# Kernel tuning notes

Measured on AMD Instinct MI355X. Metric: run time of the kernel, lower is better.

Reference implementation:

```python
import jax, jax.numpy as jnp
import numpy as np

# dims: batch, token counts, feature dims, hidden d, glimpses
B, VN, QN, AN = 16, 96, 96, 96
VD = QD = AD = 256
HD, G = 128, 2
W_STD = 0.02


def setup_inputs() -> dict:
    key = jax.random.key(0)
    ks = jax.random.split(key, 24)
    f32 = jnp.float32
    def w(k, shape):
        return jax.random.normal(k, shape, f32) * W_STD
    return {
        'v': jax.random.normal(ks[0], (B, VN, VD), f32),
        'q': jax.random.normal(ks[1], (B, QN, QD), f32),
        'a': jax.random.normal(ks[2], (B, AN, AD), f32),
        # TCNet tucker projections (FCNet: Linear + ReLU)
        'Wvt': w(ks[3], (VD, HD)), 'bvt': jnp.zeros((HD,), f32),
        'Wqt': w(ks[4], (QD, HD)), 'bqt': jnp.zeros((HD,), f32),
        'Wat': w(ks[5], (AD, HD)), 'bat': jnp.zeros((HD,), f32),
        # trilinear core mapping shared hidden dim -> glimpses
        'Wg': w(ks[6], (HD, G)),
        # value projections (plain Linear, *_dim -> h_dim)
        'Wvp': w(ks[7], (VD, HD)), 'bvp': jnp.zeros((HD,), f32),
        'Wqp': w(ks[8], (QD, HD)), 'bqp': jnp.zeros((HD,), f32),
        'Wap': w(ks[9], (AD, HD)), 'bap': jnp.zeros((HD,), f32),
        # residual updates (glimpse*h_dim -> *_dim)
        'Wvu': w(ks[10], (G * HD, VD)), 'bvu': jnp.zeros((VD,), f32),
        'Wqu': w(ks[11], (G * HD, QD)), 'bqu': jnp.zeros((QD,), f32),
        'Wau': w(ks[12], (G * HD, AD)), 'bau': jnp.zeros((AD,), f32),
    }


def reference(v, q, a,
              Wvt, bvt, Wqt, bqt, Wat, bat, Wg,
              Wvp, bvp, Wqp, bqp, Wap, bap,
              Wvu, bvu, Wqu, bqu, Wau, bau):
    b = v.shape[0]
    # --- TCNet (reconstructed trilinear scorer): tucker proj + rank-1 core ---
    vt = jax.nn.relu(v @ Wvt + bvt)               # [b, vn, h]
    qt = jax.nn.relu(q @ Wqt + bqt)               # [b, qn, h]
    at = jax.nn.relu(a @ Wat + bat)               # [b, an, h]
    logits = jnp.einsum('bvh,bqh,bah,hg->bvqag', vt, qt, at, Wg)
    z = vt.sum(1) * qt.sum(1) * at.sum(1)         # pooled trilinear embedding [b, h]
    # --- mask padded v tokens (rows whose abs-sum is 0), softmax over v*q*a ---
    mask = (jnp.abs(v).sum(2) == 0)[:, :, None, None, None]
    logits = jnp.where(mask, -jnp.inf, logits)
    p = jax.nn.softmax(logits.reshape(b, -1, G), axis=1).reshape(logits.shape)
    # --- value projections + broadcast-sum combinations ---
    vp = v @ Wvp + bvp                            # [b, vn, d]
    qp = q @ Wqp + bqp                            # [b, qn, d]
    ap = a @ Wap + bap                            # [b, an, d]
    qa = qp[:, :, None, :] + ap[:, None, :, :]    # [b, qn, an, d]
    va = vp[:, :, None, :] + ap[:, None, :, :]    # [b, vn, an, d]
    vq = vp[:, :, None, :] + qp[:, None, :, :]    # [b, vn, qn, d]
    # --- three attended contractions + residual linear updates (eval: no dropout) ---
    c_v = jnp.einsum('bvqag,bqad->bvdg', p, qa)
    c_v = jnp.swapaxes(c_v, 2, 3).reshape(b, v.shape[1], G * HD)  # permute(0,1,3,2).view
    updated_v = v + c_v @ Wvu + bvu
    c_q = jnp.einsum('bvqag,bvad->bqdg', p, va)
    c_q = jnp.swapaxes(c_q, 2, 3).reshape(b, q.shape[1], G * HD)
    updated_q = q + c_q @ Wqu + bqu
    c_a = jnp.einsum('bvqag,bvqd->bagd', p, vq)   # note: torch einsum emits [b,a,g,d]
    c_a = jnp.swapaxes(c_a, 2, 3).reshape(b, a.shape[1], HD * G)  # then permute(0,1,3,2).view
    updated_a = a + c_a @ Wau + bau
    return jnp.stack([updated_v, updated_q, updated_a])  # [3, b, n, dim]
```

## Files before the change

kernel.cpp:

```cpp
#include <hip/hip_runtime.h>


#define B_  16
#define N_  96
#define D_  256
#define H_  128
#define CV  4
#define NCH 24
#define PAD 136

typedef _Float16 f16x8 __attribute__((ext_vector_type(8)));
typedef float f32x4_t  __attribute__((ext_vector_type(4)));

__device__ __forceinline__ float bf2f(unsigned short u) {
    union { unsigned u32; float f; } x;
    x.u32 = ((unsigned)u) << 16;
    return x.f;
}

__global__ __launch_bounds__(256) void k_proj(
    const float* __restrict__ v, const float* __restrict__ q,
    const float* __restrict__ a,
    const float* __restrict__ Wvt, const float* __restrict__ bvt,
    const float* __restrict__ Wqt, const float* __restrict__ bqt,
    const float* __restrict__ Wat, const float* __restrict__ bat,
    const float* __restrict__ Wvp, const float* __restrict__ bvp,
    const float* __restrict__ Wqp, const float* __restrict__ bqp,
    const float* __restrict__ Wap, const float* __restrict__ bap,
    const float* __restrict__ Wg,
    _Float16* __restrict__ vtg_o, _Float16* __restrict__ qt_o,
    _Float16* __restrict__ at_o,
    float* __restrict__ vp_o, float* __restrict__ qp_o, float* __restrict__ ap_o)
{
    int wg = blockIdx.x;
    int tc = wg % 8, b = (wg / 8) & 15, p = wg / 128;
    const float* xs_[6] = {v, q, a, v, q, a};
    const float* Ws_[6] = {Wvt, Wqt, Wat, Wvp, Wqp, Wap};
    const float* bs_[6] = {bvt, bqt, bat, bvp, bqp, bap};

    __shared__ __align__(16) float x_l[12 * D_];

    int tid = threadIdx.x;
    int t0 = tc * 12;
    const float* x = xs_[p] + (size_t)(b * N_ + t0) * D_;
    for (int i = tid; i < 768; i += 256)
        ((float4*)x_l)[i] = ((const float4*)x)[i];
    __syncthreads();

    int d = tid & 127, tg = tid >> 7;
    const float* W = Ws_[p];
    float bias = bs_[p][d];
    float acc[6];
#pragma unroll
    for (int t = 0; t < 6; t++) acc[t] = bias;

    for (int kb = 0; kb < 32; kb++) {
        int k = kb * 8;
        float w0 = W[(k + 0) * H_ + d], w1 = W[(k + 1) * H_ + d];
        float w2 = W[(k + 2) * H_ + d], w3 = W[(k + 3) * H_ + d];
        float w4 = W[(k + 4) * H_ + d], w5 = W[(k + 5) * H_ + d];
        float w6 = W[(k + 6) * H_ + d], w7 = W[(k + 7) * H_ + d];
#pragma unroll
        for (int t = 0; t < 6; t++) {
            int lt = tg * 6 + t;
            float4 xa = *(const float4*)&x_l[lt * D_ + k];
            float4 xb = *(const float4*)&x_l[lt * D_ + k + 4];
            acc[t] += xa.x * w0 + xa.y * w1 + xa.z * w2 + xa.w * w3
                    + xb.x * w4 + xb.y * w5 + xb.z * w6 + xb.w * w7;
        }
    }

    int trow = b * N_ + t0 + tg * 6;
    if (p == 0) {
        float wg0 = Wg[d * 2 + 0], wg1 = Wg[d * 2 + 1];
#pragma unroll
        for (int t = 0; t < 6; t++) {
            float r = fmaxf(acc[t], 0.f);
            _Float16* vg = vtg_o + (size_t)(trow + t) * 2 * H_;
            vg[d]      = (_Float16)(r * wg0);
            vg[H_ + d] = (_Float16)(r * wg1);
        }
    } else if (p < 3) {
        _Float16* o = (p == 1) ? qt_o : at_o;
#pragma unroll
        for (int t = 0; t < 6; t++)
            o[(trow + t) * H_ + d] = (_Float16)fmaxf(acc[t], 0.f);
    } else {
        float* outs[3] = {vp_o, qp_o, ap_o};
        float* o = outs[p - 3];
#pragma unroll
        for (int t = 0; t < 6; t++) o[(trow + t) * H_ + d] = acc[t];
    }
}

__global__ __launch_bounds__(256) void k_logits(
    const _Float16* __restrict__ vtg, const _Float16* __restrict__ qt,
    const _Float16* __restrict__ at,
    float* __restrict__ Evq_part, float* __restrict__ Eva_part,
    unsigned short* __restrict__ E_qa_part)
{
    int bid = blockIdx.x;
    int g = bid & 1, vc = (bid >> 1) % NCH, b = bid / (2 * NCH);
    int tid = threadIdx.x;

    __shared__ __align__(16) _Float16 qt_l[N_ * PAD];
    __shared__ __align__(16) _Float16 at_l[N_ * PAD];

    const _Float16* qtb = qt + (size_t)b * N_ * H_;
    const _Float16* atb = at + (size_t)b * N_ * H_;

    for (int it = 0; it < 12; it++) {
        int i = tid + it * 256;
        int e = i * 4, t = e >> 7, h = e & 127;
        *(ushort4*)&qt_l[t * PAD + h] = *(const ushort4*)&qtb[e];
        *(ushort4*)&at_l[t * PAD + h] = *(const ushort4*)&atb[e];
    }
    __syncthreads();

    int wave = tid >> 6, lane = tid & 63, quad = lane >> 4, l15 = lane & 15;
    int qi0 = (wave >> 1) * 3, aj0 = (wave & 1) * 3;

    float eqa[3][3][4];
#pragma unroll
    for (int i = 0; i < 3; i++)
#pragma unroll
        for (int j = 0; j < 3; j++)
#pragma unroll
            for (int r = 0; r < 4; r++) eqa[i][j][r] = 0.f;

    for (int vl = 0; vl < CV; vl++) {
        int vrow = vc * CV + vl;
        const _Float16* vgp = vtg + ((size_t)(b * N_ + vrow) * 2 + g) * H_;

        f32x4_t acc[3][3];
#pragma unroll
        for (int i = 0; i < 3; i++)
#pragma unroll
            for (int j = 0; j < 3; j++)
                acc[i][j] = (f32x4_t){0.f, 0.f, 0.f, 0.f};

#pragma unroll
        for (int ks = 0; ks < 4; ks++) {
            f16x8 v8 = *(const f16x8*)&vgp[ks * 32 + quad * 8];
            f16x8 af[3], bfr[3];
#pragma unroll
            for (int i = 0; i < 3; i++)
                af[i] = *(const f16x8*)&qt_l[((qi0 + i) * 16 + l15) * PAD + ks * 32 + quad * 8];
#pragma unroll
            for (int jt = 0; jt < 3; jt++) {
                f16x8 raw = *(const f16x8*)&at_l[((aj0 + jt) * 16 + l15) * PAD + ks * 32 + quad * 8];
                bfr[jt] = raw * v8;
            }
#pragma unroll
            for (int i = 0; i < 3; i++)
#pragma unroll
                for (int jt = 0; jt < 3; jt++)
                    acc[i][jt] = __builtin_amdgcn_mfma_f32_16x16x32_f16(af[i], bfr[jt], acc[i][jt], 0, 0, 0);
        }

        float s[3][4];
        float c[3];
#pragma unroll
        for (int i = 0; i < 3; i++) {
            s[i][0] = 0.f; s[i][1] = 0.f; s[i][2] = 0.f; s[i][3] = 0.f;
        }
        c[0] = 0.f; c[1] = 0.f; c[2] = 0.f;
#pragma unroll
        for (int i = 0; i < 3; i++)
#pragma unroll
            for (int jt = 0; jt < 3; jt++) {
                float e0 = __expf(fminf(fmaxf(acc[i][jt][0], -30.f), 30.f));
                float e1 = __expf(fminf(fmaxf(acc[i][jt][1], -30.f), 30.f));
                float e2 = __expf(fminf(fmaxf(acc[i][jt][2], -30.f), 30.f));
                float e3 = __expf(fminf(fmaxf(acc[i][jt][3], -30.f), 30.f));
                eqa[i][jt][0] += e0; eqa[i][jt][1] += e1;
                eqa[i][jt][2] += e2; eqa[i][jt][3] += e3;
                s[i][0] += e0; s[i][1] += e1; s[i][2] += e2; s[i][3] += e3;
                c[jt] += e0 + e1 + e2 + e3;
            }

        float* evqp = Evq_part + ((size_t)bid * CV + vl) * 192 + (wave & 1) * 96;
#pragma unroll
        for (int i = 0; i < 3; i++) {
            float s0 = s[i][0], s1 = s[i][1], s2 = s[i][2], s3 = s[i][3];
#pragma unroll
            for (int m = 1; m < 16; m <<= 1) {
                s0 += __shfl_xor(s0, m); s1 += __shfl_xor(s1, m);
                s2 += __shfl_xor(s2, m); s3 += __shfl_xor(s3, m);
            }
            if (l15 == 0) {
                int qr = (qi0 + i) * 16 + quad * 4;
                evqp[qr + 0] = s0; evqp[qr + 1] = s1;
                evqp[qr + 2] = s2; evqp[qr + 3] = s3;
            }
        }
        float* evap = Eva_part + ((size_t)bid * CV + vl) * 192 + (wave >> 1) * 96;
#pragma unroll
        for (int jt = 0; jt < 3; jt++) {
            float cs = c[jt];
            cs += __shfl_xor(cs, 16);
            cs += __shfl_xor(cs, 32);
            if (lane < 16) evap[(aj0 + jt) * 16 + l15] = cs;
        }
    }

    unsigned short* Pp = E_qa_part + (size_t)bid * 9216;
#pragma unroll
    for (int i = 0; i < 3; i++)
#pragma unroll
        for (int jt = 0; jt < 3; jt++)
#pragma unroll
            for (int r = 0; r < 4; r++) {
                int idx = (i * 3 + jt) * 4 + r;
                union { float f; unsigned u; } x;
                x.f = eqa[i][jt][r];
                unsigned rr = x.u + 0x7fffu + ((x.u >> 16) & 1u);
                Pp[idx * 256 + tid] = (unsigned short)(rr >> 16);
            }
}

__global__ __launch_bounds__(256) void k_reduce(
    const unsigned short* __restrict__ E_qa_part, float* __restrict__ E_qa)
{
    int wg = blockIdx.x;
    int idx = wg % 36, bg = wg / 36;
    int b = bg >> 1, g = bg & 1;
    int tid = threadIdx.x;

    float s = 0.f;
    const unsigned short* Pp = E_qa_part + ((size_t)(b * 2 * NCH + g)) * 9216 + idx * 256 + tid;
#pragma unroll
    for (int vc = 0; vc < NCH; vc++) s += bf2f(Pp[(size_t)vc * 2 * 9216]);

    int wave = tid >> 6, lane = tid & 63, quad = lane >> 4, l15 = lane & 15;
    int qi0 = (wave >> 1) * 3, aj0 = (wave & 1) * 3;
    int i = idx / 12, jt = (idx / 4) % 3, r = idx & 3;
    int qq = (qi0 + i) * 16 + quad * 4 + r;
    int aa = (aj0 + jt) * 16 + l15;
    E_qa[(size_t)bg * 9216 + qq * 96 + aa] = s;
}

__global__ __launch_bounds__(256) void k_merge(
    const float* __restrict__ Evq_part, const float* __restrict__ Eva_part,
    float* __restrict__ E_vq, float* __restrict__ E_va, float* __restrict__ Zinv)
{
    int b = blockIdx.x >> 1, g = blockIdx.x & 1;
    int tid = threadIdx.x;
    float z = 0.f;
    for (int i = tid; i < 9216; i += 256) {
        int vrow = i / 96, col = i - vrow * 96;
        int vc = vrow / CV, vl = vrow - vc * CV;
        size_t pb = ((size_t)(b * 2 * NCH + vc * 2 + g) * CV + vl) * 192;
        float s1 = Evq_part[pb + col] + Evq_part[pb + 96 + col];
        E_vq[(b * 2 + g) * 9216 + i] = s1;
        z += s1;
        float s2 = Eva_part[pb + col] + Eva_part[pb + 96 + col];
        E_va[(b * 2 + g) * 9216 + i] = s2;
    }
    __shared__ float red[256];
    red[tid] = z;
    __syncthreads();
    for (int s = 128; s > 0; s >>= 1) {
        if (tid < s) red[tid] += red[tid + s];
        __syncthreads();
    }
    if (tid == 0) Zinv[b * 2 + g] = 1.f / fmaxf(red[0], 1e-30f);
}

__global__ __launch_bounds__(256) void k_ctx(
    const float* __restrict__ E_vq, const float* __restrict__ E_va,
    const float* __restrict__ E_qa,
    const float* __restrict__ vp, const float* __restrict__ qp,
    const float* __restrict__ ap, const float* __restrict__ Zinv,
    float* __restrict__ out)
{
    int wg = blockIdx.x;
    int tc = wg % 6, g = (wg / 6) & 1, b = (wg / 12) & 15, o = wg / 192;
    int tid = threadIdx.x;
    __shared__ __align__(16) float E1l[16 * 100];
    __shared__ __align__(16) float E2l[16 * 100];
    int t0 = tc * 16;
    const float* Evq = E_vq + (b * 2 + g) * 9216;
    const float* Eva = E_va + (b * 2 + g) * 9216;
    const float* Eqa = E_qa + (b * 2 + g) * 9216;

    if (o == 0) {
        for (int i = tid; i < 1536; i += 256) {
            int t = i / 96, j = i - t * 96;
            E1l[t * 100 + j] = Evq[(t0 + t) * 96 + j];
            E2l[t * 100 + j] = Eva[(t0 + t) * 96 + j];
        }
    } else if (o == 1) {
        for (int i = tid; i < 1536; i += 256) {
            int t = i & 15, j = i >> 4;
            E1l[t * 100 + j] = Evq[j * 96 + t0 + t];
        }
        for (int i = tid; i < 1536; i += 256) {
            int t = i / 96, j = i - t * 96;
            E2l[t * 100 + j] = Eqa[(t0 + t) * 96 + j];
        }
    } else {
        for (int i = tid; i < 1536; i += 256) {
            int t = i & 15, j = i >> 4;
            E1l[t * 100 + j] = Eva[j * 96 + t0 + t];
            E2l[t * 100 + j] = Eqa[j * 96 + t0 + t];
        }
    }
    __syncthreads();

    const float* P1 = ((o == 0) ? qp : vp) + b * N_ * H_;
    const float* P2 = ((o == 2) ? qp : ap) + b * N_ * H_;
    int d = tid & 127, tg = tid >> 7;
    float acc[8] = {0.f, 0.f, 0.f, 0.f, 0.f, 0.f, 0.f, 0.f};
    for (int jb = 0; jb < 24; jb++) {
        int j4 = jb * 4;
        float p10 = P1[(j4 + 0) * H_ + d], p11 = P1[(j4 + 1) * H_ + d];
        float p12 = P1[(j4 + 2) * H_ + d], p13 = P1[(j4 + 3) * H_ + d];
        float p20 = P2[(j4 + 0) * H_ + d], p21 = P2[(j4 + 1) * H_ + d];
        float p22 = P2[(j4 + 2) * H_ + d], p23 = P2[(j4 + 3) * H_ + d];
#pragma unroll
        for (int t8 = 0; t8 < 8; t8++) {
            int t = tg * 8 + t8;
            float4 e1 = *(const float4*)&E1l[t * 100 + j4];
            float4 e2 = *(const float4*)&E2l[t * 100 + j4];
            acc[t8] += e1.x * p10 + e1.y * p11 + e1.z * p12 + e1.w * p13
                     + e2.x * p20 + e2.y * p21 + e2.z * p22 + e2.w * p23;
        }
    }
    float zi = Zinv[b * 2 + g];
    float* ob = out + (size_t)((o * B_ + b) * N_) * 256;
#pragma unroll
    for (int t8 = 0; t8 < 8; t8++) {
        int T = t0 + tg * 8 + t8;
        int col = (o == 2) ? (d * 2 + g) : (g * 128 + d);
        ob[T * 256 + col] = acc[t8] * zi;
    }
}

__global__ __launch_bounds__(256) void k_update(
    const float* __restrict__ v, const float* __restrict__ q,
    const float* __restrict__ a,
    const float* __restrict__ Wvu, const float* __restrict__ bvu,
    const float* __restrict__ Wqu, const float* __restrict__ bqu,
    const float* __restrict__ Wau, const float* __restrict__ bau,
    float* __restrict__ out)
{
    int wg = blockIdx.x;
    int tc = wg % 12, b = (wg / 12) & 15, o = wg / 192;
    int tid = threadIdx.x;
    const float* xs_[3] = {v, q, a};
    const float* Ws_[3] = {Wvu, Wqu, Wau};
    const float* bs_[3] = {bvu, bqu, bau};
    int t0 = tc * 8;

    __shared__ __align__(16) float c_l[8 * 256];
    float* cbase = out + (size_t)((o * B_ + b) * N_ + t0) * 256;
    for (int i = tid; i < 2048; i += 256) c_l[i] = cbase[i];
    __syncthreads();

    const float* W = Ws_[o];
    const float* x = xs_[o] + (size_t)(b * N_ + t0) * 256;
    float bias = bs_[o][tid];
    float acc[8];
#pragma unroll
    for (int t = 0; t < 8; t++) acc[t] = bias + x[t * 256 + tid];

    for (int kb = 0; kb < 64; kb++) {
        int k = kb * 4;
        float w0 = W[(k + 0) * 256 + tid];
        float w1 = W[(k + 1) * 256 + tid];
        float w2 = W[(k + 2) * 256 + tid];
        float w3 = W[(k + 3) * 256 + tid];
#pragma unroll
        for (int t = 0; t < 8; t++) {
            float4 c4 = *(const float4*)&c_l[t * 256 + k];
            acc[t] += c4.x * w0 + c4.y * w1 + c4.z * w2 + c4.w * w3;
        }
    }
#pragma unroll
    for (int t = 0; t < 8; t++) cbase[t * 256 + tid] = acc[t];
}

extern "C" void kernel_launch(void* const* d_in, const int* in_sizes, int n_in,
                              void* d_out, int out_size, void* d_ws, size_t ws_size,
                              hipStream_t stream)
{
    const float* v   = (const float*)d_in[0];
    const float* q   = (const float*)d_in[1];
    const float* a   = (const float*)d_in[2];
    const float* Wvt = (const float*)d_in[3];
    const float* bvt = (const float*)d_in[4];
    const float* Wqt = (const float*)d_in[5];
    const float* bqt = (const float*)d_in[6];
    const float* Wat = (const float*)d_in[7];
    const float* bat = (const float*)d_in[8];
    const float* Wg  = (const float*)d_in[9];
    const float* Wvp = (const float*)d_in[10];
    const float* bvp = (const float*)d_in[11];
    const float* Wqp = (const float*)d_in[12];
    const float* bqp = (const float*)d_in[13];
    const float* Wap = (const float*)d_in[14];
    const float* bap = (const float*)d_in[15];
    const float* Wvu = (const float*)d_in[16];
    const float* bvu = (const float*)d_in[17];
    const float* Wqu = (const float*)d_in[18];
    const float* bqu = (const float*)d_in[19];
    const float* Wau = (const float*)d_in[20];
    const float* bau = (const float*)d_in[21];

    char* ws = (char*)d_ws;
    size_t off = 0;
    auto alloc = [&](size_t bytes) {
        char* p = ws + off;
        off += (bytes + 255) & ~(size_t)255;
        return (void*)p;
    };
    _Float16* vtg = (_Float16*)alloc((size_t)B_ * N_ * 2 * H_ * 2);
    _Float16* qt  = (_Float16*)alloc((size_t)B_ * N_ * H_ * 2);
    _Float16* at  = (_Float16*)alloc((size_t)B_ * N_ * H_ * 2);
    float* vpb  = (float*)alloc((size_t)B_ * N_ * H_ * 4);
    float* qpb  = (float*)alloc((size_t)B_ * N_ * H_ * 4);
    float* apb  = (float*)alloc((size_t)B_ * N_ * H_ * 4);
    float* E_vq = (float*)alloc((size_t)B_ * 2 * 9216 * 4);
    float* E_va = (float*)alloc((size_t)B_ * 2 * 9216 * 4);
    float* E_qa = (float*)alloc((size_t)B_ * 2 * 9216 * 4);
    float* Zinv = (float*)alloc(256);
    float* Evq_part = (float*)alloc((size_t)768 * CV * 192 * 4);
    float* Eva_part = (float*)alloc((size_t)768 * CV * 192 * 4);
    unsigned short* E_qa_part =
        (unsigned short*)alloc((size_t)B_ * NCH * 2 * 9216 * 2);

    k_proj<<<768, 256, 0, stream>>>(v, q, a, Wvt, bvt, Wqt, bqt, Wat, bat,
                                    Wvp, bvp, Wqp, bqp, Wap, bap, Wg,
                                    vtg, qt, at, vpb, qpb, apb);
    k_logits<<<B_ * NCH * 2, 256, 0, stream>>>(vtg, qt, at,
                                               Evq_part, Eva_part, E_qa_part);
    k_reduce<<<1152, 256, 0, stream>>>(E_qa_part, E_qa);
    k_merge<<<32, 256, 0, stream>>>(Evq_part, Eva_part, E_vq, E_va, Zinv);
    k_ctx<<<576, 256, 0, stream>>>(E_vq, E_va, E_qa, vpb, qpb, apb, Zinv,
                                   (float*)d_out);
    k_update<<<576, 256, 0, stream>>>(v, q, a, Wvu, bvu, Wqu, bqu, Wau, bau,
                                      (float*)d_out);
}
```

Baseline: 206.1 us.

## Fuse reduce/merge kernels and fuse context contraction into residual update

Merges k_reduce and k_merge into a single k_mid launch that branches on block index. Fuses k_ctx with k_update so each block computes the context for its 8 tokens across both glimpses into shared memory and immediately applies the residual linear layer. This removes two launches and the global round-trip of the context tensor through the output buffer. In exchange, each k_ctxup block now does both contractions serially with a smaller token tile, and the P1/P2 loads are repeated across more blocks.

```diff
diff --git a/kernel.cpp b/kernel.cpp
--- a/kernel.cpp
+++ b/kernel.cpp
@@ -219,125 +219,58 @@
             }
 }
 
-__global__ __launch_bounds__(256) void k_reduce(
-    const unsigned short* __restrict__ E_qa_part, float* __restrict__ E_qa)
+__global__ __launch_bounds__(256) void k_mid(
+    const unsigned short* __restrict__ E_qa_part,
+    const float* __restrict__ Evq_part, const float* __restrict__ Eva_part,
+    float* __restrict__ E_qa, float* __restrict__ E_vq,
+    float* __restrict__ E_va, float* __restrict__ Zinv)
 {
     int wg = blockIdx.x;
-    int idx = wg % 36, bg = wg / 36;
-    int b = bg >> 1, g = bg & 1;
     int tid = threadIdx.x;
-
-    float s = 0.f;
-    const unsigned short* Pp = E_qa_part + ((size_t)(b * 2 * NCH + g)) * 9216 + idx * 256 + tid;
-#pragma unroll
-    for (int vc = 0; vc < NCH; vc++) s += bf2f(Pp[(size_t)vc * 2 * 9216]);
-
-    int wave = tid >> 6, lane = tid & 63, quad = lane >> 4, l15 = lane & 15;
-    int qi0 = (wave >> 1) * 3, aj0 = (wave & 1) * 3;
-    int i = idx / 12, jt = (idx / 4) % 3, r = idx & 3;
-    int qq = (qi0 + i) * 16 + quad * 4 + r;
-    int aa = (aj0 + jt) * 16 + l15;
-    E_qa[(size_t)bg * 9216 + qq * 96 + aa] = s;
-}
-
-__global__ __launch_bounds__(256) void k_merge(
-    const float* __restrict__ Evq_part, const float* __restrict__ Eva_part,
-    float* __restrict__ E_vq, float* __restrict__ E_va, float* __restrict__ Zinv)
-{
-    int b = blockIdx.x >> 1, g = blockIdx.x & 1;
-    int tid = threadIdx.x;
-    float z = 0.f;
-    for (int i = tid; i < 9216; i += 256) {
-        int vrow = i / 96, col = i - vrow * 96;
-        int vc = vrow / CV, vl = vrow - vc * CV;
-        size_t pb = ((size_t)(b * 2 * NCH + vc * 2 + g) * CV + vl) * 192;
-        float s1 = Evq_part[pb + col] + Evq_part[pb + 96 + col];
-        E_vq[(b * 2 + g) * 9216 + i] = s1;
-        z += s1;
-        float s2 = Eva_part[pb + col] + Eva_part[pb + 96 + col];
-        E_va[(b * 2 + g) * 9216 + i] = s2;
-    }
-    __shared__ float red[256];
-    red[tid] = z;
-    __syncthreads();
-    for (int s = 128; s > 0; s >>= 1) {
-        if (tid < s) red[tid] += red[tid + s];
+    if (wg < 1152) {
+        int idx = wg % 36, bg = wg / 36;
+        int b = bg >> 1, g = bg & 1;
+        float s = 0.f;
+        const unsigned short* Pp = E_qa_part + ((size_t)(b * 2 * NCH + g)) * 9216 + idx * 256 + tid;
+#pragma unroll
+        for (int vc = 0; vc < NCH; vc++) s += bf2f(Pp[(size_t)vc * 2 * 9216]);
+
+        int wave = tid >> 6, lane = tid & 63, quad = lane >> 4, l15 = lane & 15;
+        int qi0 = (wave >> 1) * 3, aj0 = (wave & 1) * 3;
+        int i = idx / 12, jt = (idx / 4) % 3, r = idx & 3;
+        int qq = (qi0 + i) * 16 + quad * 4 + r;
+        int aa = (aj0 + jt) * 16 + l15;
+        E_qa[(size_t)bg * 9216 + qq * 96 + aa] = s;
+    } else {
+        int bg = wg - 1152;
+        int b = bg >> 1, g = bg & 1;
+        float z = 0.f;
+        for (int i = tid; i < 9216; i += 256) {
+            int vrow = i / 96, col = i - vrow * 96;
+            int vc = vrow / CV, vl = vrow - vc * CV;
+            size_t pb = ((size_t)(b * 2 * NCH + vc * 2 + g) * CV + vl) * 192;
+            float s1 = Evq_part[pb + col] + Evq_part[pb + 96 + col];
+            E_vq[(b * 2 + g) * 9216 + i] = s1;
+            z += s1;
+            float s2 = Eva_part[pb + col] + Eva_part[pb + 96 + col];
+            E_va[(b * 2 + g) * 9216 + i] = s2;
+        }
+        __shared__ float red[256];
+        red[tid] = z;
         __syncthreads();
-    }
-    if (tid == 0) Zinv[b * 2 + g] = 1.f / fmaxf(red[0], 1e-30f);
-}
-
-__global__ __launch_bounds__(256) void k_ctx(
+        for (int s = 128; s > 0; s >>= 1) {
+            if (tid < s) red[tid] += red[tid + s];
+            __syncthreads();
+        }
+        if (tid == 0) Zinv[b * 2 + g] = 1.f / fmaxf(red[0], 1e-30f);
+    }
+}
+
+__global__ __launch_bounds__(256) void k_ctxup(
     const float* __restrict__ E_vq, const float* __restrict__ E_va,
     const float* __restrict__ E_qa,
     const float* __restrict__ vp, const float* __restrict__ qp,
     const float* __restrict__ ap, const float* __restrict__ Zinv,
-    float* __restrict__ out)
-{
-    int wg = blockIdx.x;
-    int tc = wg % 6, g = (wg / 6) & 1, b = (wg / 12) & 15, o = wg / 192;
-    int tid = threadIdx.x;
-    __shared__ __align__(16) float E1l[16 * 100];
-    __shared__ __align__(16) float E2l[16 * 100];
-    int t0 = tc * 16;
-    const float* Evq = E_vq + (b * 2 + g) * 9216;
-    const float* Eva = E_va + (b * 2 + g) * 9216;
-    const float* Eqa = E_qa + (b * 2 + g) * 9216;
-
-    if (o == 0) {
-        for (int i = tid; i < 1536; i += 256) {
-            int t = i / 96, j = i - t * 96;
-            E1l[t * 100 + j] = Evq[(t0 + t) * 96 + j];
-            E2l[t * 100 + j] = Eva[(t0 + t) * 96 + j];
-        }
-    } else if (o == 1) {
-        for (int i = tid; i < 1536; i += 256) {
-            int t = i & 15, j = i >> 4;
-            E1l[t * 100 + j] = Evq[j * 96 + t0 + t];
-        }
-        for (int i = tid; i < 1536; i += 256) {
-            int t = i / 96, j = i - t * 96;
-            E2l[t * 100 + j] = Eqa[(t0 + t) * 96 + j];
-        }
-    } else {
-        for (int i = tid; i < 1536; i += 256) {
-            int t = i & 15, j = i >> 4;
-            E1l[t * 100 + j] = Eva[j * 96 + t0 + t];
-            E2l[t * 100 + j] = Eqa[j * 96 + t0 + t];
-        }
-    }
-    __syncthreads();
-
-    const float* P1 = ((o == 0) ? qp : vp) + b * N_ * H_;
-    const float* P2 = ((o == 2) ? qp : ap) + b * N_ * H_;
-    int d = tid & 127, tg = tid >> 7;
-    float acc[8] = {0.f, 0.f, 0.f, 0.f, 0.f, 0.f, 0.f, 0.f};
-    for (int jb = 0; jb < 24; jb++) {
-        int j4 = jb * 4;
-        float p10 = P1[(j4 + 0) * H_ + d], p11 = P1[(j4 + 1) * H_ + d];
-        float p12 = P1[(j4 + 2) * H_ + d], p13 = P1[(j4 + 3) * H_ + d];
-        float p20 = P2[(j4 + 0) * H_ + d], p21 = P2[(j4 + 1) * H_ + d];
-        float p22 = P2[(j4 + 2) * H_ + d], p23 = P2[(j4 + 3) * H_ + d];
-#pragma unroll
-        for (int t8 = 0; t8 < 8; t8++) {
-            int t = tg * 8 + t8;
-            float4 e1 = *(const float4*)&E1l[t * 100 + j4];
-            float4 e2 = *(const float4*)&E2l[t * 100 + j4];
-            acc[t8] += e1.x * p10 + e1.y * p11 + e1.z * p12 + e1.w * p13
-                     + e2.x * p20 + e2.y * p21 + e2.z * p22 + e2.w * p23;
-        }
-    }
-    float zi = Zinv[b * 2 + g];
-    float* ob = out + (size_t)((o * B_ + b) * N_) * 256;
-#pragma unroll
-    for (int t8 = 0; t8 < 8; t8++) {
-        int T = t0 + tg * 8 + t8;
-        int col = (o == 2) ? (d * 2 + g) : (g * 128 + d);
-        ob[T * 256 + col] = acc[t8] * zi;
-    }
-}
-
-__global__ __launch_bounds__(256) void k_update(
     const float* __restrict__ v, const float* __restrict__ q,
     const float* __restrict__ a,
     const float* __restrict__ Wvu, const float* __restrict__ bvu,
@@ -348,16 +281,57 @@
     int wg = blockIdx.x;
     int tc = wg % 12, b = (wg / 12) & 15, o = wg / 192;
     int tid = threadIdx.x;
+    int t0 = tc * 8;
+
+    __shared__ __align__(16) float E1l[2][8 * 100];
+    __shared__ __align__(16) float E2l[2][8 * 100];
+    __shared__ __align__(16) float c_l[8 * 256];
+
+    for (int i = tid; i < 1536; i += 256) {
+        int g2 = i / 768, rem = i - g2 * 768;
+        int t = rem / 96, j = rem - t * 96;
+        const float* Evq = E_vq + (b * 2 + g2) * 9216;
+        const float* Eva = E_va + (b * 2 + g2) * 9216;
+        const float* Eqa = E_qa + (b * 2 + g2) * 9216;
+        float e1, e2;
+        if (o == 0)      { e1 = Evq[(t0 + t) * 96 + j]; e2 = Eva[(t0 + t) * 96 + j]; }
+        else if (o == 1) { e1 = Evq[j * 96 + t0 + t];   e2 = Eqa[(t0 + t) * 96 + j]; }
+        else             { e1 = Eva[j * 96 + t0 + t];   e2 = Eqa[j * 96 + t0 + t]; }
+        E1l[g2][t * 100 + j] = e1;
+        E2l[g2][t * 100 + j] = e2;
+    }
+    __syncthreads();
+
+    {
+        int d = tid & 127, g2 = tid >> 7;
+        const float* P1 = ((o == 0) ? qp : vp) + b * N_ * H_;
+        const float* P2 = ((o == 2) ? qp : ap) + b * N_ * H_;
+        float acc[8] = {0.f, 0.f, 0.f, 0.f, 0.f, 0.f, 0.f, 0.f};
+        for (int jb = 0; jb < 24; jb++) {
+            int j4 = jb * 4;
+            float p10 = P1[(j4 + 0) * H_ + d], p11 = P1[(j4 + 1) * H_ + d];
+            float p12 = P1[(j4 + 2) * H_ + d], p13 = P1[(j4 + 3) * H_ + d];
+            float p20 = P2[(j4 + 0) * H_ + d], p21 = P2[(j4 + 1) * H_ + d];
+            float p22 = P2[(j4 + 2) * H_ + d], p23 = P2[(j4 + 3) * H_ + d];
+#pragma unroll
+            for (int t8 = 0; t8 < 8; t8++) {
+                float4 e1 = *(const float4*)&E1l[g2][t8 * 100 + j4];
+                float4 e2 = *(const float4*)&E2l[g2][t8 * 100 + j4];
+                acc[t8] += e1.x * p10 + e1.y * p11 + e1.z * p12 + e1.w * p13
+                         + e2.x * p20 + e2.y * p21 + e2.z * p22 + e2.w * p23;
+            }
+        }
+        float zi = Zinv[b * 2 + g2];
+        int col = (o == 2) ? (d * 2 + g2) : (g2 * 128 + d);
+#pragma unroll
+        for (int t8 = 0; t8 < 8; t8++)
+            c_l[t8 * 256 + col] = acc[t8] * zi;
+    }
+    __syncthreads();
+
     const float* xs_[3] = {v, q, a};
     const float* Ws_[3] = {Wvu, Wqu, Wau};
     const float* bs_[3] = {bvu, bqu, bau};
-    int t0 = tc * 8;
-
-    __shared__ __align__(16) float c_l[8 * 256];
-    float* cbase = out + (size_t)((o * B_ + b) * N_ + t0) * 256;
-    for (int i = tid; i < 2048; i += 256) c_l[i] = cbase[i];
-    __syncthreads();
-
     const float* W = Ws_[o];
     const float* x = xs_[o] + (size_t)(b * N_ + t0) * 256;
     float bias = bs_[o][tid];
@@ -377,8 +351,9 @@
             acc[t] += c4.x * w0 + c4.y * w1 + c4.z * w2 + c4.w * w3;
         }
     }
-#pragma unroll
-    for (int t = 0; t < 8; t++) cbase[t * 256 + tid] = acc[t];
+    float* ob = out + (size_t)((o * B_ + b) * N_ + t0) * 256;
+#pragma unroll
+    for (int t = 0; t < 8; t++) ob[t * 256 + tid] = acc[t];
 }
 
 extern "C" void kernel_launch(void* const* d_in, const int* in_sizes, int n_in,
@@ -435,10 +410,9 @@
                                     vtg, qt, at, vpb, qpb, apb);
     k_logits<<<B_ * NCH * 2, 256, 0, stream>>>(vtg, qt, at,
                                                Evq_part, Eva_part, E_qa_part);
-    k_reduce<<<1152, 256, 0, stream>>>(E_qa_part, E_qa);
-    k_merge<<<32, 256, 0, stream>>>(Evq_part, Eva_part, E_vq, E_va, Zinv);
-    k_ctx<<<576, 256, 0, stream>>>(E_vq, E_va, E_qa, vpb, qpb, apb, Zinv,
-                                   (float*)d_out);
-    k_update<<<576, 256, 0, stream>>>(v, q, a, Wvu, bvu, Wqu, bqu, Wau, bau,
-                                      (float*)d_out);
-}
+    k_mid<<<1184, 256, 0, stream>>>(E_qa_part, Evq_part, Eva_part,
+                                    E_qa, E_vq, E_va, Zinv);
+    k_ctxup<<<576, 256, 0, stream>>>(E_vq, E_va, E_qa, vpb, qpb, apb, Zinv,
+                                     v, q, a, Wvu, bvu, Wqu, bqu, Wau, bau,
+                                     (float*)d_out);
+}
```

Result: faster. 199.3 us (-3.3%).
